# Optimization experiments

Hardware: AMD Instinct MI355X
Metric: run time of the kernel (lower is better)

Reference implementation:

```python
import jax, jax.numpy as jnp
import numpy as np

B, S, DM, H = 4, 2048, 512, 8
HD = DM // H


def setup_inputs() -> dict:
    key = jax.random.key(0)
    ks = jax.random.split(key, 12)
    x = jax.random.normal(ks[0], (B, S, DM), dtype=jnp.float32)
    # causal lower-triangular mask [B, S, S]
    mask = jnp.broadcast_to(jnp.tril(jnp.ones((S, S), dtype=jnp.int32)), (B, S, S))
    # sorted irregular day offsets (trading-day-like), in days
    days_offset = jnp.sort(
        jax.random.uniform(ks[1], (B, S), dtype=jnp.float32) * 3000.0, axis=-1
    )
    scale = 1.0 / np.sqrt(DM)
    Wq = jax.random.normal(ks[2], (DM, DM), dtype=jnp.float32) * scale
    bq = jnp.zeros((DM,), dtype=jnp.float32)
    Wk = jax.random.normal(ks[3], (DM, DM), dtype=jnp.float32) * scale
    bk = jnp.zeros((DM,), dtype=jnp.float32)
    Wv = jax.random.normal(ks[4], (DM, DM), dtype=jnp.float32) * scale
    bv = jnp.zeros((DM,), dtype=jnp.float32)
    Wo = jax.random.normal(ks[5], (DM, DM), dtype=jnp.float32) * scale
    bo = jnp.zeros((DM,), dtype=jnp.float32)
    decay_rate = jnp.float32(0.1)
    return {
        "x": x, "mask": mask, "days_offset": days_offset,
        "Wq": Wq, "bq": bq, "Wk": Wk, "bk": bk,
        "Wv": Wv, "bv": bv, "Wo": Wo, "bo": bo,
        "decay_rate": decay_rate,
    }


def reference(x, mask, days_offset, Wq, bq, Wk, bk, Wv, bv, Wo, bo, decay_rate):
    b, s, _ = x.shape
    # projections (torch Linear: x @ W.T + b), split heads -> [b, h, s, hd]
    def proj(W, bias):
        return (x @ W.T + bias).reshape(b, s, H, HD).transpose(0, 2, 1, 3)
    q, k, v = proj(Wq, bq), proj(Wk, bk), proj(Wv, bv)
    scores = jnp.einsum("bhqd,bhkd->bhqk", q, k) / jnp.sqrt(jnp.float32(HD))
    # temporal decay: exp(-rate * |t_i - t_j|), broadcast over heads
    dist = jnp.abs(days_offset[:, :, None] - days_offset[:, None, :])  # [b,s,s]
    decay = jnp.exp(-decay_rate * dist)
    scores = scores * decay[:, None, :, :]
    scores = jnp.where(mask[:, None, :, :] == 0, -jnp.inf, scores)
    attn = jax.nn.softmax(scores, axis=-1)  # dropout p=0 (eval)
    out = jnp.einsum("bhqk,bhkd->bhqd", attn, v)
    out = out.transpose(0, 2, 1, 3).reshape(b, s, DM)
    return out @ Wo.T + bo
```

## Files before the change

### kernel.cpp

```cpp
#include <hip/hip_runtime.h>
#include <hip/hip_fp16.h>


#define S_LEN 2048
#define DMODEL 512
#define NH 8
#define HD 64

typedef _Float16 half8 __attribute__((ext_vector_type(8)));
typedef _Float16 half4 __attribute__((ext_vector_type(4)));
typedef float floatx4 __attribute__((ext_vector_type(4)));

__device__ __forceinline__ void gload16(const _Float16* g, _Float16* l) {
    __builtin_amdgcn_global_load_lds(
        (const __attribute__((address_space(1))) void*)g,
        (__attribute__((address_space(3))) void*)l, 16, 0, 0);
}

__device__ __forceinline__ half8 cvt8(float4 a, float4 b) {
    half8 h;
    h[0] = (_Float16)a.x; h[1] = (_Float16)a.y; h[2] = (_Float16)a.z; h[3] = (_Float16)a.w;
    h[4] = (_Float16)b.x; h[5] = (_Float16)b.y; h[6] = (_Float16)b.z; h[7] = (_Float16)b.w;
    return h;
}

__device__ __forceinline__ void stage_f32(
    const float* __restrict__ src, _Float16* __restrict__ dstbase,
    int row, int sw, int lane7, int kcol)
{
    const float* p = src + (size_t)row * DMODEL + kcol + sw * 8;
    float4 a = *(const float4*)p;
    float4 b = *(const float4*)(p + 4);
    *(half8*)(dstbase + row * 64 + lane7 * 8) = cvt8(a, b);
}

__global__ __launch_bounds__(256) void qkv_gemm(
    const float* __restrict__ x,
    const float* __restrict__ Wq, const float* __restrict__ Wk, const float* __restrict__ Wv,
    const float* __restrict__ bq, const float* __restrict__ bk, const float* __restrict__ bv,
    _Float16* __restrict__ outh)
{
    __shared__ _Float16 As[2][128 * 64];
    __shared__ _Float16 Ws[2][128 * 64];
    const int t = threadIdx.x;
    const int bm = blockIdx.x, bn = blockIdx.y, z = blockIdx.z;
    const float* Wp = (z == 0) ? Wq : (z == 1) ? Wk : Wv;
    const float* bias = (z == 0) ? bq : (z == 1) ? bk : bv;
    const int w = t >> 6, lane = t & 63, l15 = lane & 15, quad = lane >> 4;
    const int wrow = (w >> 1) * 64, wcol = (w & 1) * 64;
    const int lrow = lane >> 3, lane7 = lane & 7;
    const int sw = lane7 ^ lrow;
    const float* xb = x  + (size_t)(bm * 128) * DMODEL;
    const float* Wb = Wp + (size_t)(bn * 128) * DMODEL;

    auto stage = [&](int kb, int buf) {
        #pragma unroll
        for (int i = 0; i < 4; ++i) {
            int row = w * 32 + i * 8 + lrow;
            stage_f32(xb, As[buf], row, sw, lane7, kb * 64);
            stage_f32(Wb, Ws[buf], row, sw, lane7, kb * 64);
        }
    };

    floatx4 acc[4][4] = {};
    stage(0, 0);
    for (int kb = 0; kb < 8; ++kb) {
        const int buf = kb & 1;
        __syncthreads();
        if (kb < 7) stage(kb + 1, buf ^ 1);
        #pragma unroll
        for (int kk = 0; kk < 2; ++kk) {
            half8 xf[4], wf[4];
            #pragma unroll
            for (int mt = 0; mt < 4; ++mt)
                xf[mt] = *(const half8*)(&As[buf][(wrow + mt * 16 + l15) * 64 + (((quad + 4 * kk) ^ (l15 & 7)) * 8)]);
            #pragma unroll
            for (int nt = 0; nt < 4; ++nt)
                wf[nt] = *(const half8*)(&Ws[buf][(wcol + nt * 16 + l15) * 64 + (((quad + 4 * kk) ^ (l15 & 7)) * 8)]);
            if (z == 2) {
                #pragma unroll
                for (int mt = 0; mt < 4; ++mt)
                    #pragma unroll
                    for (int nt = 0; nt < 4; ++nt)
                        acc[mt][nt] = __builtin_amdgcn_mfma_f32_16x16x32_f16(xf[mt], wf[nt], acc[mt][nt], 0, 0, 0);
            } else {
                #pragma unroll
                for (int nt = 0; nt < 4; ++nt)
                    #pragma unroll
                    for (int mt = 0; mt < 4; ++mt)
                        acc[nt][mt] = __builtin_amdgcn_mfma_f32_16x16x32_f16(wf[nt], xf[mt], acc[nt][mt], 0, 0, 0);
            }
        }
    }

    if (z == 2) {
        #pragma unroll
        for (int mt = 0; mt < 4; ++mt)
            #pragma unroll
            for (int nt = 0; nt < 4; ++nt) {
                int n = bn * 128 + wcol + nt * 16 + l15;
                float bvv = bias[n];
                int m0 = bm * 128 + wrow + mt * 16 + quad * 4;
                int b = m0 >> 11, s0 = m0 & 2047;
                int hh = n >> 6, hd = n & 63;
                half4 hv;
                #pragma unroll
                for (int r = 0; r < 4; ++r) hv[r] = (_Float16)(acc[mt][nt][r] + bvv);
                *(half4*)(outh + (size_t)2 * (8192 * 512) +
                          ((size_t)(b * NH + hh) * HD + hd) * S_LEN + s0) = hv;
            }
    } else {
        #pragma unroll
        for (int nt = 0; nt < 4; ++nt)
            #pragma unroll
            for (int mt = 0; mt < 4; ++mt) {
                int n0 = bn * 128 + wcol + nt * 16 + quad * 4;
                float4 b4 = *(const float4*)(bias + n0);
                int m = bm * 128 + wrow + mt * 16 + l15;
                int b = m >> 11, s = m & 2047;
                int hh = n0 >> 6, hd0 = n0 & 63;
                half4 hv;
                hv[0] = (_Float16)(acc[nt][mt][0] + b4.x);
                hv[1] = (_Float16)(acc[nt][mt][1] + b4.y);
                hv[2] = (_Float16)(acc[nt][mt][2] + b4.z);
                hv[3] = (_Float16)(acc[nt][mt][3] + b4.w);
                *(half4*)(outh + (size_t)z * (8192 * 512) +
                          ((size_t)(b * NH + hh) * S_LEN + s) * HD + hd0) = hv;
            }
    }
}

__global__ __launch_bounds__(256) void out_gemm(
    const _Float16* __restrict__ A, const float* __restrict__ Wo,
    const float* __restrict__ bo, float* __restrict__ outf)
{
    __shared__ _Float16 As[2][64 * 64];
    __shared__ _Float16 Ws[2][128 * 64];
    const int t = threadIdx.x;
    const int bm = blockIdx.x, bn = blockIdx.y;
    const int w = t >> 6, lane = t & 63, l15 = lane & 15, quad = lane >> 4;
    const int wn = w * 32;
    const int lrow = lane >> 3, lane7 = lane & 7;
    const int sw = lane7 ^ lrow;
    const _Float16* Ab = A  + (size_t)(bm * 64) * DMODEL;
    const float*    Wb = Wo + (size_t)(bn * 128) * DMODEL;

    auto stage = [&](int kb, int buf) {
        #pragma unroll
        for (int i = 0; i < 2; ++i) {
            int row = (w * 2 + i) * 8 + lrow;
            gload16(Ab + (size_t)row * DMODEL + kb * 64 + sw * 8, &As[buf][row * 64]);
        }
        #pragma unroll
        for (int i = 0; i < 4; ++i)
            stage_f32(Wb, Ws[buf], w * 32 + i * 8 + lrow, sw, lane7, kb * 64);
    };

    floatx4 acc[2][4] = {};
    stage(0, 0);
    for (int kb = 0; kb < 8; ++kb) {
        const int buf = kb & 1;
        __syncthreads();
        if (kb < 7) stage(kb + 1, buf ^ 1);
        #pragma unroll
        for (int kk = 0; kk < 2; ++kk) {
            half8 wf[2], af[4];
            #pragma unroll
            for (int nt = 0; nt < 2; ++nt)
                wf[nt] = *(const half8*)(&Ws[buf][(wn + nt * 16 + l15) * 64 + (((quad + 4 * kk) ^ (l15 & 7)) * 8)]);
            #pragma unroll
            for (int mt = 0; mt < 4; ++mt)
                af[mt] = *(const half8*)(&As[buf][(mt * 16 + l15) * 64 + (((quad + 4 * kk) ^ (l15 & 7)) * 8)]);
            #pragma unroll
            for (int nt = 0; nt < 2; ++nt)
                #pragma unroll
                for (int mt = 0; mt < 4; ++mt)
                    acc[nt][mt] = __builtin_amdgcn_mfma_f32_16x16x32_f16(wf[nt], af[mt], acc[nt][mt], 0, 0, 0);
        }
    }

    #pragma unroll
    for (int nt = 0; nt < 2; ++nt)
        #pragma unroll
        for (int mt = 0; mt < 4; ++mt) {
            int n0 = bn * 128 + wn + nt * 16 + quad * 4;
            float4 b4 = *(const float4*)(bo + n0);
            int m = bm * 64 + mt * 16 + l15;
            float4 v;
            v.x = acc[nt][mt][0] + b4.x; v.y = acc[nt][mt][1] + b4.y;
            v.z = acc[nt][mt][2] + b4.z; v.w = acc[nt][mt][3] + b4.w;
            *(float4*)(outf + (size_t)m * DMODEL + n0) = v;
        }
}

__global__ __launch_bounds__(256, 2) void attn_k(
    const _Float16* __restrict__ Qh, const _Float16* __restrict__ Kh,
    const _Float16* __restrict__ Vt, const float* __restrict__ days,
    const float* __restrict__ rate_p, _Float16* __restrict__ Ah)
{
    __shared__ _Float16 Ks[2][64 * 64];
    __shared__ _Float16 Vs[2][64 * 64];
    __shared__ float    eks[2][64];
    __shared__ _Float16 Ps[4][16 * 64];

    const int h = blockIdx.x, pr = blockIdx.y, b = blockIdx.z;
    const int t = threadIdx.x, w = t >> 6, lane = t & 63, l15 = lane & 15, quad = lane >> 4;
    const float rate = rate_p[0];
    const size_t bhoff = (size_t)(b * NH + h) * (size_t)(S_LEN * HD);
    const _Float16* Qb = Qh + bhoff;
    const _Float16* Kb = Kh + bhoff;
    const _Float16* Vb = Vt + bhoff;
    const float* daysb = days + b * S_LEN;
    const int lrow = lane >> 3, sw = (lane & 7) ^ lrow;
    const int e7 = l15 & 7;

    auto stage = [&](int kt, int buf) {
        #pragma unroll
        for (int i = 0; i < 2; ++i) {
            int grp = w * 2 + i;
            int row = grp * 8 + lrow;
            gload16(Kb + (size_t)(kt * 64 + row) * HD + sw * 8, &Ks[buf][grp * 512]);
            gload16(Vb + (size_t)row * S_LEN + kt * 64 + sw * 8, &Vs[buf][grp * 512]);
        }
        if (w == 0) {
            float tk0 = daysb[kt * 64];
            float d = daysb[kt * 64 + lane];
            eks[buf][lane] = __expf(fminf(rate * (d - tk0), 80.f));
        }
    };

    auto run_phase = [&](int j, int par0, int nextj) -> int {
        const int qg = j * 64 + w * 16 + l15;
        half8 qf0 = *(const half8*)(Qb + (size_t)qg * HD + quad * 8);
        half8 qf1 = *(const half8*)(Qb + (size_t)qg * HD + 32 + quad * 8);
        const float tq = daysb[qg];
        floatx4 oacc[4] = {};
        float lacc = 0.f;

        floatx4 scA[4], scB[4], eqA[4], eqB[4];
        half8 vfA[4][2], vfB[4][2];

        auto load_tile = [&](int kt, int par, floatx4 (&sc)[4],
                             half8 (&vf)[4][2], floatx4 (&eqk)[4]) {
            half8 kf[4][2];
            #pragma unroll
            for (int c = 0; c < 4; ++c)
                #pragma unroll
                for (int kk = 0; kk < 2; ++kk)
                    kf[c][kk] = *(const half8*)(&Ks[par][(c * 16 + l15) * 64 + (((quad + 4 * kk) ^ e7) * 8)]);
            #pragma unroll
            for (int c = 0; c < 4; ++c) {
                floatx4 z4 = {};
                z4 = __builtin_amdgcn_mfma_f32_16x16x32_f16(kf[c][0], qf0, z4, 0, 0, 0);
                sc[c] = __builtin_amdgcn_mfma_f32_16x16x32_f16(kf[c][1], qf1, z4, 0, 0, 0);
            }
            #pragma unroll
            for (int s4 = 0; s4 < 4; ++s4)
                #pragma unroll
                for (int kk = 0; kk < 2; ++kk)
                    vf[s4][kk] = *(const half8*)(&Vs[par][(s4 * 16 + l15) * 64 + (((quad + 4 * kk) ^ e7) * 8)]);
            const float tk0 = daysb[kt * 64];
            const float eq = 0.125f * __expf(-rate * (tq - tk0));
            #pragma unroll
            for (int c = 0; c < 4; ++c)
                eqk[c] = eq * *(const floatx4*)(&eks[par][c * 16 + quad * 4]);
        };

        auto softmax_pv = [&](floatx4 (&sc)[4], half8 (&vf)[4][2],
                              floatx4 (&eqk)[4], bool dg, int kt) {
            #pragma unroll
            for (int c = 0; c < 4; ++c) {
                float pvv[4];
                #pragma unroll
                for (int r = 0; r < 4; ++r) {
                    float p = __expf(sc[c][r] * eqk[c][r]);
                    if (dg && (kt * 64 + c * 16 + quad * 4 + r) > qg) p = 0.f;
                    lacc += p;
                    pvv[r] = p;
                }
                half4 hv;
                hv[0] = (_Float16)pvv[0]; hv[1] = (_Float16)pvv[1];
                hv[2] = (_Float16)pvv[2]; hv[3] = (_Float16)pvv[3];
                *(half4*)(&Ps[w][l15 * 64 + (((2 * c + (quad >> 1)) ^ e7) * 8) + (quad & 1) * 4]) = hv;
            }
            half8 pf0 = *(const half8*)(&Ps[w][l15 * 64 + ((quad ^ e7) * 8)]);
            half8 pf1 = *(const half8*)(&Ps[w][l15 * 64 + (((4 + quad) ^ e7) * 8)]);
            #pragma unroll
            for (int s4 = 0; s4 < 4; ++s4) {
                oacc[s4] = __builtin_amdgcn_mfma_f32_16x16x32_f16(vf[s4][0], pf0, oacc[s4], 0, 0, 0);
                oacc[s4] = __builtin_amdgcn_mfma_f32_16x16x32_f16(vf[s4][1], pf1, oacc[s4], 0, 0, 0);
            }
        };

        auto stage_next = [&](int kt, int par) {
            if (kt < j) stage(kt + 1, par ^ 1);
            else if (nextj >= 0) stage(0, par ^ 1);
        };

        __syncthreads();
        stage_next(0, par0);
        load_tile(0, par0, scA, vfA, eqA);

        int kt = 1;
        for (; kt + 1 <= j; kt += 2) {
            int p1 = (par0 + kt) & 1;
            __syncthreads();
            stage_next(kt, p1);
            load_tile(kt, p1, scB, vfB, eqB);
            softmax_pv(scA, vfA, eqA, false, kt - 1);
            int p2 = p1 ^ 1;
            __syncthreads();
            stage_next(kt + 1, p2);
            load_tile(kt + 1, p2, scA, vfA, eqA);
            softmax_pv(scB, vfB, eqB, false, kt);
        }
        if (kt <= j) {
            int p1 = (par0 + kt) & 1;
            __syncthreads();
            stage_next(kt, p1);
            load_tile(kt, p1, scB, vfB, eqB);
            softmax_pv(scA, vfA, eqA, false, kt - 1);
            softmax_pv(scB, vfB, eqB, true, j);
        } else {
            softmax_pv(scA, vfA, eqA, true, j);
        }

        float l = lacc;
        l += __shfl_xor(l, 16);
        l += __shfl_xor(l, 32);
        float linv = 1.0f / l;
        #pragma unroll
        for (int s4 = 0; s4 < 4; ++s4) {
            half4 hv;
            #pragma unroll
            for (int r = 0; r < 4; ++r) hv[r] = (_Float16)(oacc[s4][r] * linv);
            *(half4*)(Ah + ((size_t)(b * S_LEN) + qg) * DMODEL + h * HD + s4 * 16 + quad * 4) = hv;
        }
        return (par0 + j + 1) & 1;
    };

    const int j0 = pr, j1 = 31 - pr;
    stage(0, 0);
    int p1 = run_phase(j0, 0, j1);
    run_phase(j1, p1, -1);
}

extern "C" void kernel_launch(void* const* d_in, const int* in_sizes, int n_in,
                              void* d_out, int out_size, void* d_ws, size_t ws_size,
                              hipStream_t stream)
{
    const float* x    = (const float*)d_in[0];
    const float* days = (const float*)d_in[2];
    const float* Wq   = (const float*)d_in[3];
    const float* bq   = (const float*)d_in[4];
    const float* Wk   = (const float*)d_in[5];
    const float* bk   = (const float*)d_in[6];
    const float* Wv   = (const float*)d_in[7];
    const float* bv   = (const float*)d_in[8];
    const float* Wo   = (const float*)d_in[9];
    const float* bo   = (const float*)d_in[10];
    const float* rate = (const float*)d_in[11];
    float* out = (float*)d_out;

    _Float16* Qh = (_Float16*)d_ws;
    _Float16* Kh = Qh + 4194304;
    _Float16* Vh = Kh + 4194304;
    _Float16* Ah = Vh + 4194304;

    dim3 g0(64, 4, 3);
    qkv_gemm<<<g0, 256, 0, stream>>>(x, Wq, Wk, Wv, bq, bk, bv, Qh);

    dim3 ga(NH, 16, 4);
    attn_k<<<ga, 256, 0, stream>>>(Qh, Kh, Vh, days, rate, Ah);

    dim3 g1(128, 4, 1);
    out_gemm<<<g1, 256, 0, stream>>>(Ah, Wo, bo, out);
}
```

Measured before the change: 204.8 us.

## Restructure attention: per-wave independent causal tiles with direct global K/V loads

```diff
diff --git a/kernel.cpp b/kernel.cpp
--- a/kernel.cpp
+++ b/kernel.cpp
@@ -193,156 +193,147 @@
         }
 }
 
-__global__ __launch_bounds__(256, 2) void attn_k(
+__global__ __launch_bounds__(512, 2) void attn_k(
     const _Float16* __restrict__ Qh, const _Float16* __restrict__ Kh,
     const _Float16* __restrict__ Vt, const float* __restrict__ days,
     const float* __restrict__ rate_p, _Float16* __restrict__ Ah)
 {
-    __shared__ _Float16 Ks[2][64 * 64];
-    __shared__ _Float16 Vs[2][64 * 64];
-    __shared__ float    eks[2][64];
-    __shared__ _Float16 Ps[4][16 * 64];
-
-    const int h = blockIdx.x, pr = blockIdx.y, b = blockIdx.z;
-    const int t = threadIdx.x, w = t >> 6, lane = t & 63, l15 = lane & 15, quad = lane >> 4;
+    __shared__ float eks_all[2048];
+    __shared__ float tk0s[32];
+    __shared__ _Float16 Ps[16][16 * 64];
+
+    const int h = blockIdx.x, y = blockIdx.y, b = blockIdx.z;
+    const int t = threadIdx.x, w = t >> 6, lane = t & 63;
+    const int l15 = lane & 15, quad = lane >> 4, e7 = l15 & 7;
     const float rate = rate_p[0];
     const size_t bhoff = (size_t)(b * NH + h) * (size_t)(S_LEN * HD);
     const _Float16* Qb = Qh + bhoff;
     const _Float16* Kb = Kh + bhoff;
     const _Float16* Vb = Vt + bhoff;
     const float* daysb = days + b * S_LEN;
-    const int lrow = lane >> 3, sw = (lane & 7) ^ lrow;
-    const int e7 = l15 & 7;
-
-    auto stage = [&](int kt, int buf) {
-        #pragma unroll
-        for (int i = 0; i < 2; ++i) {
-            int grp = w * 2 + i;
-            int row = grp * 8 + lrow;
-            gload16(Kb + (size_t)(kt * 64 + row) * HD + sw * 8, &Ks[buf][grp * 512]);
-            gload16(Vb + (size_t)row * S_LEN + kt * 64 + sw * 8, &Vs[buf][grp * 512]);
-        }
-        if (w == 0) {
-            float tk0 = daysb[kt * 64];
-            float d = daysb[kt * 64 + lane];
-            eks[buf][lane] = __expf(fminf(rate * (d - tk0), 80.f));
-        }
+
+    {
+        int k0 = t * 4;
+        float tk0 = daysb[k0 & ~63];
+        #pragma unroll
+        for (int i = 0; i < 4; ++i) {
+            float d = daysb[k0 + i];
+            eks_all[k0 + i] = __expf(fminf(rate * (d - tk0), 80.f));
+        }
+        if (t < 32) tk0s[t] = daysb[t * 64];
+    }
+    __syncthreads();
+
+    const int wi = w & 3;
+    const int j = (w >> 2) ? (15 - y) : y;
+    const int s = 4 * j + wi;
+    const int q0 = s * 32;
+    const int nt = (s >> 1) + 1;
+
+    half8 qf[2][2];
+    #pragma unroll
+    for (int qc = 0; qc < 2; ++qc)
+        #pragma unroll
+        for (int kk = 0; kk < 2; ++kk)
+            qf[qc][kk] = *(const half8*)(Qb + (size_t)(q0 + qc * 16 + l15) * HD + kk * 32 + quad * 8);
+
+    const int   qg0 = q0 + l15,       qg1 = q0 + 16 + l15;
+    const float tq0 = daysb[qg0],     tq1 = daysb[qg1];
+
+    floatx4 oacc[2][4] = {};
+    float lacc[2] = {0.f, 0.f};
+
+    half8 kf[4][2];
+    half8 vf[4][2];
+
+    auto load_kf = [&](int kt) {
+        #pragma unroll
+        for (int c = 0; c < 4; ++c)
+            #pragma unroll
+            for (int kk = 0; kk < 2; ++kk)
+                kf[c][kk] = *(const half8*)(Kb + (size_t)(kt * 64 + c * 16 + l15) * HD + kk * 32 + quad * 8);
     };
 
-    auto run_phase = [&](int j, int par0, int nextj) -> int {
-        const int qg = j * 64 + w * 16 + l15;
-        half8 qf0 = *(const half8*)(Qb + (size_t)qg * HD + quad * 8);
-        half8 qf1 = *(const half8*)(Qb + (size_t)qg * HD + 32 + quad * 8);
-        const float tq = daysb[qg];
-        floatx4 oacc[4] = {};
-        float lacc = 0.f;
-
-        floatx4 scA[4], scB[4], eqA[4], eqB[4];
-        half8 vfA[4][2], vfB[4][2];
-
-        auto load_tile = [&](int kt, int par, floatx4 (&sc)[4],
-                             half8 (&vf)[4][2], floatx4 (&eqk)[4]) {
-            half8 kf[4][2];
-            #pragma unroll
-            for (int c = 0; c < 4; ++c)
-                #pragma unroll
-                for (int kk = 0; kk < 2; ++kk)
-                    kf[c][kk] = *(const half8*)(&Ks[par][(c * 16 + l15) * 64 + (((quad + 4 * kk) ^ e7) * 8)]);
-            #pragma unroll
-            for (int c = 0; c < 4; ++c) {
-                floatx4 z4 = {};
-                z4 = __builtin_amdgcn_mfma_f32_16x16x32_f16(kf[c][0], qf0, z4, 0, 0, 0);
-                sc[c] = __builtin_amdgcn_mfma_f32_16x16x32_f16(kf[c][1], qf1, z4, 0, 0, 0);
-            }
-            #pragma unroll
-            for (int s4 = 0; s4 < 4; ++s4)
-                #pragma unroll
-                for (int kk = 0; kk < 2; ++kk)
-                    vf[s4][kk] = *(const half8*)(&Vs[par][(s4 * 16 + l15) * 64 + (((quad + 4 * kk) ^ e7) * 8)]);
-            const float tk0 = daysb[kt * 64];
-            const float eq = 0.125f * __expf(-rate * (tq - tk0));
-            #pragma unroll
-            for (int c = 0; c < 4; ++c)
-                eqk[c] = eq * *(const floatx4*)(&eks[par][c * 16 + quad * 4]);
-        };
-
-        auto softmax_pv = [&](floatx4 (&sc)[4], half8 (&vf)[4][2],
-                              floatx4 (&eqk)[4], bool dg, int kt) {
-            #pragma unroll
-            for (int c = 0; c < 4; ++c) {
-                float pvv[4];
+    auto do_tile = [&](int kt, bool dg, bool pre) {
+        #pragma unroll
+        for (int s4 = 0; s4 < 4; ++s4)
+            #pragma unroll
+            for (int kk = 0; kk < 2; ++kk)
+                vf[s4][kk] = *(const half8*)(Vb + (size_t)(s4 * 16 + l15) * S_LEN + kt * 64 + kk * 32 + quad * 8);
+
+        floatx4 sc[2][4];
+        __builtin_amdgcn_s_setprio(1);
+        #pragma unroll
+        for (int c = 0; c < 4; ++c) {
+            floatx4 z0 = {}, z1 = {};
+            z0 = __builtin_amdgcn_mfma_f32_16x16x32_f16(kf[c][0], qf[0][0], z0, 0, 0, 0);
+            z1 = __builtin_amdgcn_mfma_f32_16x16x32_f16(kf[c][0], qf[1][0], z1, 0, 0, 0);
+            sc[0][c] = __builtin_amdgcn_mfma_f32_16x16x32_f16(kf[c][1], qf[0][1], sc[0][c] = z0, 0, 0, 0);
+            sc[1][c] = __builtin_amdgcn_mfma_f32_16x16x32_f16(kf[c][1], qf[1][1], sc[1][c] = z1, 0, 0, 0);
+        }
+        __builtin_amdgcn_s_setprio(0);
+
+        if (pre) load_kf(kt + 1);
+
+        const float tk0 = tk0s[kt];
+        const float eq0 = 0.125f * __expf(-rate * (tq0 - tk0));
+        const float eq1 = 0.125f * __expf(-rate * (tq1 - tk0));
+        #pragma unroll
+        for (int c = 0; c < 4; ++c) {
+            floatx4 ek4 = *(const floatx4*)(&eks_all[kt * 64 + c * 16 + quad * 4]);
+            #pragma unroll
+            for (int qc = 0; qc < 2; ++qc) {
+                const float eqv = qc ? eq1 : eq0;
+                const int   qg  = qc ? qg1 : qg0;
+                float pv[4];
                 #pragma unroll
                 for (int r = 0; r < 4; ++r) {
-                    float p = __expf(sc[c][r] * eqk[c][r]);
+                    float p = __expf(sc[qc][c][r] * (eqv * ek4[r]));
                     if (dg && (kt * 64 + c * 16 + quad * 4 + r) > qg) p = 0.f;
-                    lacc += p;
-                    pvv[r] = p;
+                    lacc[qc] += p;
+                    pv[r] = p;
                 }
                 half4 hv;
-                hv[0] = (_Float16)pvv[0]; hv[1] = (_Float16)pvv[1];
-                hv[2] = (_Float16)pvv[2]; hv[3] = (_Float16)pvv[3];
-                *(half4*)(&Ps[w][l15 * 64 + (((2 * c + (quad >> 1)) ^ e7) * 8) + (quad & 1) * 4]) = hv;
-            }
-            half8 pf0 = *(const half8*)(&Ps[w][l15 * 64 + ((quad ^ e7) * 8)]);
-            half8 pf1 = *(const half8*)(&Ps[w][l15 * 64 + (((4 + quad) ^ e7) * 8)]);
+                hv[0] = (_Float16)pv[0]; hv[1] = (_Float16)pv[1];
+                hv[2] = (_Float16)pv[2]; hv[3] = (_Float16)pv[3];
+                *(half4*)(&Ps[w * 2 + qc][l15 * 64 + (((2 * c + (quad >> 1)) ^ e7) * 8) + (quad & 1) * 4]) = hv;
+            }
+        }
+
+        __builtin_amdgcn_s_setprio(1);
+        #pragma unroll
+        for (int qc = 0; qc < 2; ++qc) {
+            half8 pf0 = *(const half8*)(&Ps[w * 2 + qc][l15 * 64 + ((quad ^ e7) * 8)]);
+            half8 pf1 = *(const half8*)(&Ps[w * 2 + qc][l15 * 64 + (((4 + quad) ^ e7) * 8)]);
             #pragma unroll
             for (int s4 = 0; s4 < 4; ++s4) {
-                oacc[s4] = __builtin_amdgcn_mfma_f32_16x16x32_f16(vf[s4][0], pf0, oacc[s4], 0, 0, 0);
-                oacc[s4] = __builtin_amdgcn_mfma_f32_16x16x32_f16(vf[s4][1], pf1, oacc[s4], 0, 0, 0);
-            }
-        };
-
-        auto stage_next = [&](int kt, int par) {
-            if (kt < j) stage(kt + 1, par ^ 1);
-            else if (nextj >= 0) stage(0, par ^ 1);
-        };
-
-        __syncthreads();
-        stage_next(0, par0);
-        load_tile(0, par0, scA, vfA, eqA);
-
-        int kt = 1;
-        for (; kt + 1 <= j; kt += 2) {
-            int p1 = (par0 + kt) & 1;
-            __syncthreads();
-            stage_next(kt, p1);
-            load_tile(kt, p1, scB, vfB, eqB);
-            softmax_pv(scA, vfA, eqA, false, kt - 1);
-            int p2 = p1 ^ 1;
-            __syncthreads();
-            stage_next(kt + 1, p2);
-            load_tile(kt + 1, p2, scA, vfA, eqA);
-            softmax_pv(scB, vfB, eqB, false, kt);
-        }
-        if (kt <= j) {
-            int p1 = (par0 + kt) & 1;
-            __syncthreads();
-            stage_next(kt, p1);
-            load_tile(kt, p1, scB, vfB, eqB);
-            softmax_pv(scA, vfA, eqA, false, kt - 1);
-            softmax_pv(scB, vfB, eqB, true, j);
-        } else {
-            softmax_pv(scA, vfA, eqA, true, j);
-        }
-
-        float l = lacc;
+                oacc[qc][s4] = __builtin_amdgcn_mfma_f32_16x16x32_f16(vf[s4][0], pf0, oacc[qc][s4], 0, 0, 0);
+                oacc[qc][s4] = __builtin_amdgcn_mfma_f32_16x16x32_f16(vf[s4][1], pf1, oacc[qc][s4], 0, 0, 0);
+            }
+        }
+        __builtin_amdgcn_s_setprio(0);
+    };
+
+    load_kf(0);
+    for (int kt = 0; kt < nt - 1; ++kt)
+        do_tile(kt, false, true);
+    do_tile(nt - 1, true, false);
+
+    #pragma unroll
+    for (int qc = 0; qc < 2; ++qc) {
+        float l = lacc[qc];
         l += __shfl_xor(l, 16);
         l += __shfl_xor(l, 32);
         float linv = 1.0f / l;
+        const int qg = qc ? qg1 : qg0;
         #pragma unroll
         for (int s4 = 0; s4 < 4; ++s4) {
             half4 hv;
             #pragma unroll
-            for (int r = 0; r < 4; ++r) hv[r] = (_Float16)(oacc[s4][r] * linv);
+            for (int r = 0; r < 4; ++r) hv[r] = (_Float16)(oacc[qc][s4][r] * linv);
             *(half4*)(Ah + ((size_t)(b * S_LEN) + qg) * DMODEL + h * HD + s4 * 16 + quad * 4) = hv;
         }
-        return (par0 + j + 1) & 1;
-    };
-
-    const int j0 = pr, j1 = 31 - pr;
-    stage(0, 0);
-    int p1 = run_phase(j0, 0, j1);
-    run_phase(j1, p1, -1);
+    }
 }
 
 extern "C" void kernel_launch(void* const* d_in, const int* in_sizes, int n_in,
@@ -370,8 +361,8 @@
     dim3 g0(64, 4, 3);
     qkv_gemm<<<g0, 256, 0, stream>>>(x, Wq, Wk, Wv, bq, bk, bv, Qh);
 
-    dim3 ga(NH, 16, 4);
-    attn_k<<<ga, 256, 0, stream>>>(Qh, Kh, Vh, days, rate, Ah);
+    dim3 ga(NH, 8, 4);
+    attn_k<<<ga, 512, 0, stream>>>(Qh, Kh, Vh, days, rate, Ah);
 
     dim3 g1(128, 4, 1);
     out_gemm<<<g1, 256, 0, stream>>>(Ah, Wo, bo, out);
```

Result: slower. 230.7 us (+12.6%).
